# Kernel optimization log

Hardware: AMD Instinct MI355X
Metric: run time of the kernel (lower is better)

The kernel has to match this reference:

```python
import jax, jax.numpy as jnp
import numpy as np

N_NODES = 100000


def gcn_conv(x, edge_index, W, b):
    # PyG GCNConv: add self-loops, symmetric normalization D^-1/2 (A+I) D^-1/2
    src, dst = edge_index[0], edge_index[1]
    n = x.shape[0]
    ones = jnp.ones(src.shape[0], dtype=x.dtype)
    deg = jax.ops.segment_sum(ones, dst, num_segments=n) + 1.0  # +1 self-loop
    dinv = jax.lax.rsqrt(deg)
    h = x @ W  # transform first (smaller gather traffic when out_dim < in_dim)
    norm = dinv[src] * dinv[dst]  # [E]
    msg = h[src] * norm[:, None]  # [E, out]
    agg = jax.ops.segment_sum(msg, dst, num_segments=n)
    agg = agg + h * (dinv * dinv)[:, None]  # self-loop contribution
    return agg + b


def setup_inputs() -> dict:
    key = jax.random.key(0)
    k = jax.random.split(key, 8)
    feature_size = 128
    n_edges = 3200000
    x = jax.random.normal(k[0], (N_NODES, feature_size), dtype=jnp.float32)
    edge_index = jax.random.randint(k[1], (2, n_edges), 0, N_NODES, dtype=jnp.int64)
    # Glorot-ish params
    W1 = jax.random.normal(k[2], (feature_size, 64), dtype=jnp.float32) / np.sqrt(feature_size)
    b1 = jnp.zeros((64,), dtype=jnp.float32)
    W2 = jax.random.normal(k[3], (64, 128), dtype=jnp.float32) / np.sqrt(64)
    b2 = jnp.zeros((128,), dtype=jnp.float32)
    Wfc = jax.random.normal(k[4], (128, 1), dtype=jnp.float32) / np.sqrt(128)
    bfc = jnp.zeros((1,), dtype=jnp.float32)
    return {"x": x, "edge_index": edge_index, "W1": W1, "b1": b1,
            "W2": W2, "b2": b2, "Wfc": Wfc, "bfc": bfc}


def reference(x, edge_index, W1, b1, W2, b2, Wfc, bfc):
    h = jax.nn.relu(gcn_conv(x, edge_index, W1, b1))
    h = jax.nn.relu(gcn_conv(h, edge_index, W2, b2))
    return h @ Wfc + bfc  # [N, 1]
```

## Files before the change

### kernel.cpp

```cpp
#include <hip/hip_runtime.h>
#include <hip/hip_fp16.h>

#define NN 100000
#define NBIN 256
#define RANGE 391
#define CAP 16384
#define CAPL 16384

typedef _Float16 f16x8 __attribute__((ext_vector_type(8)));
typedef float f32x4 __attribute__((ext_vector_type(4)));

__global__ __launch_bounds__(256) void k_binA(const int* __restrict__ ei_lo,
                                              int E, int* __restrict__ g_bincnt,
                                              unsigned* __restrict__ binbuf) {
    constexpr int ITER = 16;
    __shared__ int cnt[NBIN], basep[NBIN], pos[NBIN];
    __shared__ int s_is64;
    const int t = threadIdx.x;
    const int base = blockIdx.x * (256 * ITER);

    cnt[t] = 0; pos[t] = 0;
    if (t == 0) {
        const unsigned* u = (const unsigned*)ei_lo;
        int is64 = 1;
        for (int i = 0; i < 64; ++i)
            if (u[2 * i + 1] != 0u) { is64 = 0; break; }
        s_is64 = is64;
    }
    __syncthreads();
    const int s = s_is64 ? 2 : 1;

    unsigned pk[ITER];
    int bn[ITER];
#pragma unroll
    for (int i = 0; i < ITER; ++i) {
        int e = base + i * 256 + t;
        if (e < E) {
            int src = __builtin_nontemporal_load(&ei_lo[(long long)s * e]);
            int dst = __builtin_nontemporal_load(&ei_lo[(long long)s * (E + e)]);
            int b = dst / RANGE;
            bn[i] = b;
            pk[i] = ((unsigned)(dst - b * RANGE) << 17) | (unsigned)src;
            atomicAdd(&cnt[b], 1);
        } else bn[i] = -1;
    }
    __syncthreads();
    basep[t] = atomicAdd(&g_bincnt[t], cnt[t]);
    __syncthreads();
#pragma unroll
    for (int i = 0; i < ITER; ++i) {
        if (bn[i] >= 0) {
            int r = atomicAdd(&pos[bn[i]], 1);
            binbuf[(long long)bn[i] * CAP + basep[bn[i]] + r] = pk[i];
        }
    }
}

__global__ __launch_bounds__(512) void k_build(const unsigned* __restrict__ binbuf,
                                               const int* __restrict__ g_bincnt,
                                               int* __restrict__ row_ptr,
                                               float* __restrict__ dinv,
                                               int* __restrict__ csr, int n, int E) {
    __shared__ unsigned ebuf[CAPL];
    __shared__ int cnt[512];
    __shared__ int ssum[256];
    __shared__ int pref[NBIN];
    const int t = threadIdx.x;
    const int bin = blockIdx.x;
    const int lo = bin * RANGE;
    const int rn = min(RANGE, n - lo);
    const int nE = min(g_bincnt[bin], CAPL);
    const unsigned* __restrict__ src = binbuf + (long long)bin * CAP;

    cnt[t] = 0;
    if (t < NBIN) pref[t] = g_bincnt[t];
    __syncthreads();

    for (int i = t; i < nE; i += 512) {
        unsigned e = src[i];
        ebuf[i] = e;
        atomicAdd(&cnt[(int)(e >> 17)], 1);
    }
    __syncthreads();

    for (int off = 1; off < NBIN; off <<= 1) {
        int add = (t >= off && t < NBIN) ? pref[t - off] : 0;
        __syncthreads();
        if (t < NBIN) pref[t] += add;
        __syncthreads();
    }
    const int bstart = (bin > 0) ? pref[bin - 1] : 0;

    int a = 0, bcnt = 0;
    if (t < 256) { a = cnt[2 * t]; bcnt = cnt[2 * t + 1]; ssum[t] = a + bcnt; }
    __syncthreads();
    for (int off = 1; off < 256; off <<= 1) {
        int add = (t >= off && t < 256) ? ssum[t - off] : 0;
        __syncthreads();
        if (t < 256) ssum[t] += add;
        __syncthreads();
    }
    if (t < 256) {
        int prev = (t > 0) ? ssum[t - 1] : 0;
        cnt[2 * t] = prev;
        cnt[2 * t + 1] = prev + a;
        if (2 * t < rn) {
            row_ptr[lo + 2 * t] = bstart + prev;
            dinv[lo + 2 * t] = rsqrtf((float)a + 1.f);
        }
        if (2 * t + 1 < rn) {
            row_ptr[lo + 2 * t + 1] = bstart + prev + a;
            dinv[lo + 2 * t + 1] = rsqrtf((float)bcnt + 1.f);
        }
    }
    if (bin == NBIN - 1 && t == 0) row_ptr[n] = E;
    __syncthreads();

    for (int i = t; i < nE; i += 512) {
        unsigned e = ebuf[i];
        int slot = bstart + atomicAdd(&cnt[(int)(e >> 17)], 1);
        csr[slot] = (int)(e & 0x1FFFFu);
    }
}

__global__ __launch_bounds__(256) void k_gemm1(const float* __restrict__ X,
                                               const float* __restrict__ W,
                                               const float* __restrict__ dinv,
                                               __half* __restrict__ H, int n) {
    constexpr int K = 128, C = 64, RPT = 2;
    constexpr int CG = C / 4, RS = 256 / CG, RT = RS * RPT, XS = K + 4;
    __shared__ float Ws[K * C];
    __shared__ float Xs[RT * XS];
    const int t = threadIdx.x;

    for (int i = t * 4; i < K * C; i += 1024)
        *(float4*)&Ws[i] = *(const float4*)&W[i];

    const int row0 = blockIdx.x * RT;
    for (int i = t * 4; i < RT * K; i += 1024) {
        int r = i / K, k = i % K;
        int gr = row0 + r;
        float4 v = make_float4(0.f, 0.f, 0.f, 0.f);
        if (gr < n) v = *(const float4*)&X[(long long)gr * K + k];
        *(float4*)&Xs[r * XS + k] = v;
    }
    __syncthreads();

    const int cg = t % CG, rs = t / CG;
    float acc[RPT][4];
#pragma unroll
    for (int i = 0; i < RPT; ++i)
#pragma unroll
        for (int j = 0; j < 4; ++j) acc[i][j] = 0.f;

#pragma unroll 2
    for (int k4 = 0; k4 < K / 4; ++k4) {
        float4 xv[RPT];
#pragma unroll
        for (int i = 0; i < RPT; ++i)
            xv[i] = *(float4*)&Xs[(rs * RPT + i) * XS + k4 * 4];
#pragma unroll
        for (int j = 0; j < 4; ++j) {
            float4 w = *(float4*)&Ws[(k4 * 4 + j) * C + cg * 4];
#pragma unroll
            for (int i = 0; i < RPT; ++i) {
                float xvj = (&xv[i].x)[j];
                acc[i][0] = fmaf(xvj, w.x, acc[i][0]);
                acc[i][1] = fmaf(xvj, w.y, acc[i][1]);
                acc[i][2] = fmaf(xvj, w.z, acc[i][2]);
                acc[i][3] = fmaf(xvj, w.w, acc[i][3]);
            }
        }
    }
#pragma unroll
    for (int i = 0; i < RPT; ++i) {
        int gr = row0 + rs * RPT + i;
        if (gr < n) {
            float sc = dinv[gr];
            union { __half h[4]; uint2 u; } pk;
            pk.h[0] = __float2half(acc[i][0] * sc);
            pk.h[1] = __float2half(acc[i][1] * sc);
            pk.h[2] = __float2half(acc[i][2] * sc);
            pk.h[3] = __float2half(acc[i][3] * sc);
            *(uint2*)&H[(long long)gr * C + cg * 4] = pk.u;
        }
    }
}

template <bool RELU>
__global__ __launch_bounds__(256) void k_gather(const __half* __restrict__ h,
                                                const int* __restrict__ row_ptr,
                                                const int* __restrict__ csr,
                                                const float* __restrict__ dinv,
                                                const float* __restrict__ bias,
                                                __half* __restrict__ out, int n) {
    const int node = blockIdx.x * 4 + (threadIdx.x >> 6);
    if (node >= n) return;
    const int lane = threadIdx.x & 63;
    const int g = lane >> 3;
    const int fl = lane & 7;
    const float d = dinv[node];
    const int beg = row_ptr[node], end = row_ptr[node + 1];
    const int last = end - 1;
    const int zrow = n;

    uint4 su = make_uint4(0u, 0u, 0u, 0u);
    if (g == 0) su = *(const uint4*)&h[(long long)node * 64 + fl * 8];

    __half2 z = __float2half2_rn(0.f);
    __half2 acc0 = z, acc1 = z, acc2 = z, acc3 = z;

    for (int base = beg; base < end; base += 32) {
        int e0 = base + g, e1 = base + 8 + g, e2 = base + 16 + g, e3 = base + 24 + g;
        int c0 = csr[min(e0, last)];
        int c1 = csr[min(e1, last)];
        int c2 = csr[min(e2, last)];
        int c3 = csr[min(e3, last)];
        int s0 = (e0 < end) ? c0 : zrow;
        int s1 = (e1 < end) ? c1 : zrow;
        int s2 = (e2 < end) ? c2 : zrow;
        int s3 = (e3 < end) ? c3 : zrow;
        uint4 u0 = *(const uint4*)&h[(long long)s0 * 64 + fl * 8];
        uint4 u1 = *(const uint4*)&h[(long long)s1 * 64 + fl * 8];
        uint4 u2 = *(const uint4*)&h[(long long)s2 * 64 + fl * 8];
        uint4 u3 = *(const uint4*)&h[(long long)s3 * 64 + fl * 8];
        __half2 p0 = __hadd2(*(__half2*)&u0.x, *(__half2*)&u1.x);
        __half2 q0 = __hadd2(*(__half2*)&u2.x, *(__half2*)&u3.x);
        acc0 = __hadd2(acc0, __hadd2(p0, q0));
        __half2 p1 = __hadd2(*(__half2*)&u0.y, *(__half2*)&u1.y);
        __half2 q1 = __hadd2(*(__half2*)&u2.y, *(__half2*)&u3.y);
        acc1 = __hadd2(acc1, __hadd2(p1, q1));
        __half2 p2 = __hadd2(*(__half2*)&u0.z, *(__half2*)&u1.z);
        __half2 q2 = __hadd2(*(__half2*)&u2.z, *(__half2*)&u3.z);
        acc2 = __hadd2(acc2, __hadd2(p2, q2));
        __half2 p3 = __hadd2(*(__half2*)&u0.w, *(__half2*)&u1.w);
        __half2 q3 = __hadd2(*(__half2*)&u2.w, *(__half2*)&u3.w);
        acc3 = __hadd2(acc3, __hadd2(p3, q3));
    }

    float2 f0 = __half22float2(acc0);
    float2 f1 = __half22float2(acc1);
    float2 f2 = __half22float2(acc2);
    float2 f3 = __half22float2(acc3);
    float r0 = f0.x, r1 = f0.y, r2 = f1.x, r3 = f1.y;
    float r4 = f2.x, r5 = f2.y, r6 = f3.x, r7 = f3.y;
#pragma unroll
    for (int off = 8; off <= 32; off <<= 1) {
        r0 += __shfl_xor(r0, off, 64);
        r1 += __shfl_xor(r1, off, 64);
        r2 += __shfl_xor(r2, off, 64);
        r3 += __shfl_xor(r3, off, 64);
        r4 += __shfl_xor(r4, off, 64);
        r5 += __shfl_xor(r5, off, 64);
        r6 += __shfl_xor(r6, off, 64);
        r7 += __shfl_xor(r7, off, 64);
    }
    if (g == 0) {
        float2 s0 = __half22float2(*(__half2*)&su.x);
        float2 s1 = __half22float2(*(__half2*)&su.y);
        float2 s2 = __half22float2(*(__half2*)&su.z);
        float2 s3 = __half22float2(*(__half2*)&su.w);
        r0 += s0.x; r1 += s0.y; r2 += s1.x; r3 += s1.y;
        r4 += s2.x; r5 += s2.y; r6 += s3.x; r7 += s3.y;
        union { __half hh[8]; uint4 u; } o;
        if (RELU) {
            float4 bv0 = *(const float4*)&bias[fl * 8];
            float4 bv1 = *(const float4*)&bias[fl * 8 + 4];
            o.hh[0] = __float2half(fmaxf(fmaf(d, r0, bv0.x), 0.f) * d);
            o.hh[1] = __float2half(fmaxf(fmaf(d, r1, bv0.y), 0.f) * d);
            o.hh[2] = __float2half(fmaxf(fmaf(d, r2, bv0.z), 0.f) * d);
            o.hh[3] = __float2half(fmaxf(fmaf(d, r3, bv0.w), 0.f) * d);
            o.hh[4] = __float2half(fmaxf(fmaf(d, r4, bv1.x), 0.f) * d);
            o.hh[5] = __float2half(fmaxf(fmaf(d, r5, bv1.y), 0.f) * d);
            o.hh[6] = __float2half(fmaxf(fmaf(d, r6, bv1.z), 0.f) * d);
            o.hh[7] = __float2half(fmaxf(fmaf(d, r7, bv1.w), 0.f) * d);
        } else {
            o.hh[0] = __float2half(d * r0);
            o.hh[1] = __float2half(d * r1);
            o.hh[2] = __float2half(d * r2);
            o.hh[3] = __float2half(d * r3);
            o.hh[4] = __float2half(d * r4);
            o.hh[5] = __float2half(d * r5);
            o.hh[6] = __float2half(d * r6);
            o.hh[7] = __float2half(d * r7);
        }
        *(uint4*)&out[(long long)node * 64 + fl * 8] = o.u;
    }
}

__global__ __launch_bounds__(256) void k_gemm2fc(const __half* __restrict__ G,
                                                 const float* __restrict__ W2,
                                                 const float* __restrict__ b2,
                                                 const float* __restrict__ Wfc,
                                                 const float* __restrict__ bfc,
                                                 float* __restrict__ out, int n) {
    __shared__ __align__(16) _Float16 W2T[128][72];
    __shared__ float b2s[128], wfs[128];
    const int t = threadIdx.x;
    for (int i = t; i < 64 * 128; i += 256) {
        int k = i >> 7, c = i & 127;
        W2T[c][k] = (_Float16)W2[i];
    }
    if (t < 128) { b2s[t] = b2[t]; wfs[t] = Wfc[t]; }
    __syncthreads();

    const int w = t >> 6;
    const int l = t & 63;
    const int c16 = l & 15;
    const int q = l >> 4;
    const int row0 = blockIdx.x * 64 + w * 16;
    const int ar = row0 + c16;

    const _Float16* Gf = (const _Float16*)G;
    f16x8 a0 = {}, a1 = {};
    if (ar < n) {
        a0 = *(const f16x8*)&Gf[(long long)ar * 64 + q * 8];
        a1 = *(const f16x8*)&Gf[(long long)ar * 64 + 32 + q * 8];
    }

    float p0 = 0.f, p1 = 0.f, p2 = 0.f, p3 = 0.f;
#pragma unroll
    for (int ct = 0; ct < 8; ++ct) {
        f16x8 b0 = *(const f16x8*)&W2T[ct * 16 + c16][q * 8];
        f16x8 b1 = *(const f16x8*)&W2T[ct * 16 + c16][32 + q * 8];
        f32x4 acc = {0.f, 0.f, 0.f, 0.f};
        acc = __builtin_amdgcn_mfma_f32_16x16x32_f16(a0, b0, acc, 0, 0, 0);
        acc = __builtin_amdgcn_mfma_f32_16x16x32_f16(a1, b1, acc, 0, 0, 0);
        int col = ct * 16 + c16;
        float bb = b2s[col], wf = wfs[col];
        p0 += fmaxf(acc[0] + bb, 0.f) * wf;
        p1 += fmaxf(acc[1] + bb, 0.f) * wf;
        p2 += fmaxf(acc[2] + bb, 0.f) * wf;
        p3 += fmaxf(acc[3] + bb, 0.f) * wf;
    }
#pragma unroll
    for (int off = 1; off <= 8; off <<= 1) {
        p0 += __shfl_xor(p0, off, 64);
        p1 += __shfl_xor(p1, off, 64);
        p2 += __shfl_xor(p2, off, 64);
        p3 += __shfl_xor(p3, off, 64);
    }
    if (c16 == 0) {
        int row = row0 + q * 4;
        float bf = bfc[0];
        if (row < n)     out[row]     = p0 + bf;
        if (row + 1 < n) out[row + 1] = p1 + bf;
        if (row + 2 < n) out[row + 2] = p2 + bf;
        if (row + 3 < n) out[row + 3] = p3 + bf;
    }
}

extern "C" void kernel_launch(void* const* d_in, const int* in_sizes, int n_in,
                              void* d_out, int out_size, void* d_ws, size_t ws_size,
                              hipStream_t stream) {
    const float* x   = (const float*)d_in[0];
    const void*  ei  = d_in[1];
    const float* W1  = (const float*)d_in[2];
    const float* b1  = (const float*)d_in[3];
    const float* W2  = (const float*)d_in[4];
    const float* b2  = (const float*)d_in[5];
    const float* Wfc = (const float*)d_in[6];
    const float* bfc = (const float*)d_in[7];
    float* out = (float*)d_out;

    const int N = NN;
    const int E = in_sizes[1] / 2;

    char* ws = (char*)d_ws;
    size_t o = 0;
    auto carve = [&](size_t bytes) {
        char* p = ws + o;
        o = (o + bytes + 255) & ~(size_t)255;
        return p;
    };
    float*    dinv      = (float*)carve((size_t)N * 4);
    int*      row_ptr   = (int*)carve((size_t)(N + 1) * 4);
    int*      g_bincnt  = (int*)carve((size_t)NBIN * 4);
    int*      csr       = (int*)carve((size_t)E * 4);
    unsigned* binbuf    = (unsigned*)carve((size_t)NBIN * CAP * 4);
    __half*   bufA      = (__half*)carve((size_t)(N + 1) * 64 * 2);
    __half*   bufB      = (__half*)carve((size_t)(N + 1) * 64 * 2);
    __half*   bufG      = (__half*)carve((size_t)N * 64 * 2);

    const int* ei_lo = (const int*)ei;

    hipMemsetAsync(g_bincnt, 0, (size_t)NBIN * 4, stream);
    hipMemsetAsync(bufA + (size_t)N * 64, 0, 128, stream);
    hipMemsetAsync(bufB + (size_t)N * 64, 0, 128, stream);

    k_binA<<<(E + 4095) / 4096, 256, 0, stream>>>(ei_lo, E, g_bincnt, binbuf);
    k_build<<<NBIN, 512, 0, stream>>>(binbuf, g_bincnt, row_ptr, dinv, csr, N, E);

    k_gemm1<<<(N + 31) / 32, 256, 0, stream>>>(x, W1, dinv, bufA, N);
    k_gather<true><<<(N + 3) / 4, 256, 0, stream>>>(bufA, row_ptr, csr, dinv, b1, bufB, N);

    k_gather<false><<<(N + 3) / 4, 256, 0, stream>>>(bufB, row_ptr, csr, dinv, nullptr, bufG, N);
    k_gemm2fc<<<(N + 63) / 64, 256, 0, stream>>>(bufG, W2, b2, Wfc, bfc, out, N);
}
```

Baseline: 217.7 us.

## Fold zero-row memsets into binning kernel, split gather loop, use nontemporal loads

The two small memsets that zero the padding rows are replaced by stores in block 0 of the binning kernel, removing two stream operations. The gather loop is split into a fast path for full 32-edge chunks, which skips the clamping and the select against the zero row, plus a masked tail. Streaming input loads in gemm1 and gemm2fc become nontemporal to reduce cache pollution. The gains are small per item, and the extra loop code may raise register pressure.

After: 217.7 us. No clear change (+0.0%).

```diff
diff --git a/kernel.cpp b/kernel.cpp
--- a/kernel.cpp
+++ b/kernel.cpp
@@ -12,12 +12,19 @@
 
 __global__ __launch_bounds__(256) void k_binA(const int* __restrict__ ei_lo,
                                               int E, int* __restrict__ g_bincnt,
-                                              unsigned* __restrict__ binbuf) {
+                                              unsigned* __restrict__ binbuf,
+                                              __half* __restrict__ zeroA,
+                                              __half* __restrict__ zeroB) {
     constexpr int ITER = 16;
     __shared__ int cnt[NBIN], basep[NBIN], pos[NBIN];
     __shared__ int s_is64;
     const int t = threadIdx.x;
     const int base = blockIdx.x * (256 * ITER);
+
+    if (blockIdx.x == 0) {
+        if (t < 8) *(uint4*)&zeroA[t * 8] = make_uint4(0u, 0u, 0u, 0u);
+        else if (t < 16) *(uint4*)&zeroB[(t - 8) * 8] = make_uint4(0u, 0u, 0u, 0u);
+    }
 
     cnt[t] = 0; pos[t] = 0;
     if (t == 0) {
@@ -140,9 +147,9 @@
     for (int i = t * 4; i < RT * K; i += 1024) {
         int r = i / K, k = i % K;
         int gr = row0 + r;
-        float4 v = make_float4(0.f, 0.f, 0.f, 0.f);
-        if (gr < n) v = *(const float4*)&X[(long long)gr * K + k];
-        *(float4*)&Xs[r * XS + k] = v;
+        f32x4 v = {0.f, 0.f, 0.f, 0.f};
+        if (gr < n) v = __builtin_nontemporal_load((const f32x4*)&X[(long long)gr * K + k]);
+        *(f32x4*)&Xs[r * XS + k] = v;
     }
     __syncthreads();
 
@@ -201,7 +208,6 @@
     const int fl = lane & 7;
     const float d = dinv[node];
     const int beg = row_ptr[node], end = row_ptr[node + 1];
-    const int last = end - 1;
     const int zrow = n;
 
     uint4 su = make_uint4(0u, 0u, 0u, 0u);
@@ -210,7 +216,32 @@
     __half2 z = __float2half2_rn(0.f);
     __half2 acc0 = z, acc1 = z, acc2 = z, acc3 = z;
 
-    for (int base = beg; base < end; base += 32) {
+    int base = beg;
+    const int nfull = (end - beg) >> 5;
+    for (int it = 0; it < nfull; ++it, base += 32) {
+        int s0 = csr[base + g];
+        int s1 = csr[base + 8 + g];
+        int s2 = csr[base + 16 + g];
+        int s3 = csr[base + 24 + g];
+        uint4 u0 = *(const uint4*)&h[(long long)s0 * 64 + fl * 8];
+        uint4 u1 = *(const uint4*)&h[(long long)s1 * 64 + fl * 8];
+        uint4 u2 = *(const uint4*)&h[(long long)s2 * 64 + fl * 8];
+        uint4 u3 = *(const uint4*)&h[(long long)s3 * 64 + fl * 8];
+        __half2 p0 = __hadd2(*(__half2*)&u0.x, *(__half2*)&u1.x);
+        __half2 q0 = __hadd2(*(__half2*)&u2.x, *(__half2*)&u3.x);
+        acc0 = __hadd2(acc0, __hadd2(p0, q0));
+        __half2 p1 = __hadd2(*(__half2*)&u0.y, *(__half2*)&u1.y);
+        __half2 q1 = __hadd2(*(__half2*)&u2.y, *(__half2*)&u3.y);
+        acc1 = __hadd2(acc1, __hadd2(p1, q1));
+        __half2 p2 = __hadd2(*(__half2*)&u0.z, *(__half2*)&u1.z);
+        __half2 q2 = __hadd2(*(__half2*)&u2.z, *(__half2*)&u3.z);
+        acc2 = __hadd2(acc2, __hadd2(p2, q2));
+        __half2 p3 = __hadd2(*(__half2*)&u0.w, *(__half2*)&u1.w);
+        __half2 q3 = __hadd2(*(__half2*)&u2.w, *(__half2*)&u3.w);
+        acc3 = __hadd2(acc3, __hadd2(p3, q3));
+    }
+    if (base < end) {
+        const int last = end - 1;
         int e0 = base + g, e1 = base + 8 + g, e2 = base + 16 + g, e3 = base + 24 + g;
         int c0 = csr[min(e0, last)];
         int c1 = csr[min(e1, last)];
@@ -314,8 +345,8 @@
     const _Float16* Gf = (const _Float16*)G;
     f16x8 a0 = {}, a1 = {};
     if (ar < n) {
-        a0 = *(const f16x8*)&Gf[(long long)ar * 64 + q * 8];
-        a1 = *(const f16x8*)&Gf[(long long)ar * 64 + 32 + q * 8];
+        a0 = __builtin_nontemporal_load((const f16x8*)&Gf[(long long)ar * 64 + q * 8]);
+        a1 = __builtin_nontemporal_load((const f16x8*)&Gf[(long long)ar * 64 + 32 + q * 8]);
     }
 
     float p0 = 0.f, p1 = 0.f, p2 = 0.f, p3 = 0.f;
@@ -385,10 +416,10 @@
     const int* ei_lo = (const int*)ei;
 
     hipMemsetAsync(g_bincnt, 0, (size_t)NBIN * 4, stream);
-    hipMemsetAsync(bufA + (size_t)N * 64, 0, 128, stream);
-    hipMemsetAsync(bufB + (size_t)N * 64, 0, 128, stream);
-
-    k_binA<<<(E + 4095) / 4096, 256, 0, stream>>>(ei_lo, E, g_bincnt, binbuf);
+
+    k_binA<<<(E + 4095) / 4096, 256, 0, stream>>>(ei_lo, E, g_bincnt, binbuf,
+                                                  bufA + (size_t)N * 64,
+                                                  bufB + (size_t)N * 64);
     k_build<<<NBIN, 512, 0, stream>>>(binbuf, g_bincnt, row_ptr, dinv, csr, N, E);
 
     k_gemm1<<<(N + 31) / 32, 256, 0, stream>>>(x, W1, dinv, bufA, N);
```
